# Kernel optimization log

Measured on AMD Instinct MI355X. Metric: run time of the kernel, lower is better.

Reference implementation:

```python
import jax, jax.numpy as jnp
from jax import lax
import numpy as np

B, N = 8192, 4096


def thomas_algorithm(a, b, c, f):
    """Batched Thomas tridiagonal solve.
    a: (B, N-1) sub-diagonal (row i uses a[:, i-1])
    b: (B, N)   diagonal
    c: (B, N-1) super-diagonal (row i uses c[:, i])
    f: (B, N)   rhs
    returns u: (B, N) with A u = f
    """
    Bb = f.shape[0]
    zero_col = jnp.zeros((Bb, 1), dtype=f.dtype)
    a_full = jnp.concatenate([zero_col, a], axis=1)  # (B, N), a_full[:,0] unused (=0)
    c_full = jnp.concatenate([c, zero_col], axis=1)  # (B, N), c_full[:,N-1] unused (=0)

    def fwd_step(carry, inp):
        cp_prev, dp_prev = carry
        ai, bi, ci, fi = inp
        denom = bi - ai * cp_prev
        cp = ci / denom
        dp = (fi - ai * dp_prev) / denom
        return (cp, dp), (cp, dp)

    init = (jnp.zeros(Bb, dtype=f.dtype), jnp.zeros(Bb, dtype=f.dtype))
    xs = (a_full.T, b.T, c_full.T, f.T)  # scan over N, vectorized over B
    _, (cps, dps) = lax.scan(fwd_step, init, xs)

    def bwd_step(u_next, inp):
        cp, dp = inp
        u = dp - cp * u_next
        return u, u

    _, us = lax.scan(bwd_step, jnp.zeros(Bb, dtype=f.dtype), (cps, dps), reverse=True)
    return us.T  # (B, N)


def setup_inputs() -> dict:
    key = jax.random.key(0)
    k1, k2 = jax.random.split(key)
    alpha = jax.random.uniform(k1, (B, N), dtype=jnp.float32)
    f = jax.random.normal(k2, (N,), dtype=jnp.float32)
    return {"alpha": alpha, "f": f}


def reference(alpha, f):
    # f is 1D metadata -> expand to batch, matching torch forward
    f2 = jnp.broadcast_to(f[None, :], alpha.shape)
    # tridiagonal_matrix(alpha)
    a = alpha[:, :-1] ** 2
    b = jnp.maximum(5.0 + alpha ** 3, 0.01)
    c = alpha[:, 1:] ** 2 + 2.0 * alpha[:, 1:]
    u = thomas_algorithm(a, b, c, f2)
    return u
```

## Files before the change

kernel.cpp:

```cpp
#include <hip/hip_runtime.h>


namespace {
constexpr int kCH  = 32;
constexpr int kHL  = 8;
constexpr int kR   = kCH + kHL;
constexpr int kNC  = 128;
constexpr int RPW  = 8;
constexpr int THREADS = 128;
constexpr int F4PR = 69;
constexpr int ST4  = 71;
constexpr int APW4 = RPW * ST4;
constexpr int SF4  = 133;
constexpr int GHI  = 11;
}

using f4v = float __attribute__((ext_vector_type(4)));
using h2v = __fp16 __attribute__((ext_vector_type(2)));

__global__ __launch_bounds__(THREADS, 3) void thomas_v18(
    const float4* __restrict__ alpha4,
    const float4* __restrict__ f4,
    float4* __restrict__ u4)
{
  __shared__ float4 sM[2 * APW4 + SF4];

  const int bid  = blockIdx.x;
  const int pair = bid & 7;
  const int rw0  = (bid >> 3) * RPW;
  const int w    = threadIdx.x >> 6;
  const int lane = threadIdx.x & 63;
  const int j    = lane & 7;
  const int q    = lane >> 3;
  const int cw   = pair * 2 + w;

  float4* __restrict__ sA = sM + w * APW4;
  float4* __restrict__ sF = sM + 2 * APW4;

  {
    const int fb4 = pair * 128 - 3;
    #pragma unroll
    for (int it = 0; it < 3; ++it) {
      const int idx = lane + it * 64;
      if (idx < SF4) {
        int g4 = fb4 + idx;
        g4 = (g4 < 0) ? 0 : ((g4 > 1023) ? 1023 : g4);
        sF[idx] = f4[g4];
      }
    }
  }

  {
    const int cb4 = cw * 64 - 3;
    #pragma unroll 3
    for (int it = 0; it < 9; ++it) {
      int idx = lane + it * 64;
      if (idx > RPW * F4PR - 1) idx = RPW * F4PR - 1;
      const int row = idx / F4PR;
      const int c4  = idx - row * F4PR;
      int g4 = cb4 + c4;
      g4 = (g4 < 0) ? 0 : ((g4 > 1023) ? 1023 : g4);
      sA[row * ST4 + c4] = alpha4[(size_t)(rw0 + row) * 1024 + g4];
    }
  }

#define STEP(am1v, fiv)                                        \
  {                                                            \
    const float c_  = ap1 * (ap1 + 2.0f);                      \
    const float b_  = fmaxf(fmaf(a0 * a0, a0, 5.0f), 0.01f);   \
    const float dn  = fmaf(-c_, ec, b_);                       \
    const float rd  = __builtin_amdgcn_rcpf(dn);               \
    gc = (fiv - c_ * gc) * rd;                                 \
    ec = ((am1v) * (am1v)) * rd;                               \
    ap1 = a0; a0 = (am1v);                                     \
  }

  const int  kk    = cw * 8 + q;
  const bool first = (kk == 0);
  const bool last  = (kk == kNC - 1);
  const int  f4b   = first ? 3 : (q * 8 + 1);
  const int  fOff  = w * 64;
  const float4* __restrict__ A4 = sA + j * ST4;

  h2v gp_pk[kR / 2], ep_pk[kR / 2];
  float ec = 0.0f, gc = 0.0f, ap1 = 0.0f;
  const int ghi = last ? 9 : GHI;
  float4 curA = A4[f4b + ghi];
  float4 lowA = A4[f4b + ghi - 1];
  float4 fcur = sF[fOff + f4b + ghi];
  float4 flow = sF[fOff + f4b + ghi - 1];
  float a0 = curA.w;

  if (!last) {
    #pragma unroll
    for (int g = GHI; g >= 10; --g) {
      const float4 pA = A4[f4b + g - 2];
      const float4 pF = sF[fOff + f4b + g - 2];
      STEP(curA.z, fcur.w)
      STEP(curA.y, fcur.z)
      STEP(curA.x, fcur.y)
      STEP(lowA.w, fcur.x)
      curA = lowA; lowA = pA; fcur = flow; flow = pF;
    }
  }

  #pragma unroll
  for (int g = 9; g >= 0; --g) {
    int pidx = f4b + g - 2;
    if (pidx < 0) pidx = 0;
    const float4 pA = A4[pidx];
    const float4 pF = sF[fOff + pidx];
    float lw = lowA.w;
    if (g == 0 && first) lw = 0.0f;
    STEP(curA.z, fcur.w)  const float g3_ = gc, e3_ = ec;
    STEP(curA.y, fcur.z)  const float g2_ = gc, e2_ = ec;
    STEP(curA.x, fcur.y)  const float g1_ = gc, e1_ = ec;
    STEP(lw,     fcur.x)  const float g0_ = gc, e0_ = ec;
    gp_pk[2 * g + 1] = __builtin_amdgcn_cvt_pkrtz(g2_, g3_);
    gp_pk[2 * g]     = __builtin_amdgcn_cvt_pkrtz(g0_, g1_);
    ep_pk[2 * g + 1] = __builtin_amdgcn_cvt_pkrtz(e2_, e3_);
    ep_pk[2 * g]     = __builtin_amdgcn_cvt_pkrtz(e0_, e1_);
    curA = lowA; lowA = pA; fcur = flow; flow = pF;
  }

  const int tmin = first ? 0 : kHL;
  float up = 0.0f;
  float4 pk;
  #pragma unroll
  for (int t = 0; t < kR; ++t) {
    const float gpv = (float)gp_pk[t >> 1][t & 1];
    const float epv = (float)ep_pk[t >> 1][t & 1];
    const float uv = fmaf(-epv, up, gpv);
    up = uv;
    const int ph = t & 3;
    if      (ph == 0) pk.x = uv;
    else if (ph == 1) pk.y = uv;
    else if (ph == 2) pk.z = uv;
    else {
      pk.w = uv;
      if (t - 3 >= tmin && t < tmin + kCH) {
        sA[j * ST4 + q * 8 + ((t - 3 - tmin) >> 2)] = pk;
      }
    }
  }

  #pragma unroll
  for (int it = 0; it < RPW; ++it) {
    const float4 v = sA[it * ST4 + lane];
    f4v vv; vv.x = v.x; vv.y = v.y; vv.z = v.z; vv.w = v.w;
    __builtin_nontemporal_store(vv, reinterpret_cast<f4v*>(
        u4 + (size_t)(rw0 + it) * 1024 + cw * 64 + lane));
  }

#undef STEP
}

extern "C" void kernel_launch(void* const* d_in, const int* in_sizes, int n_in,
                              void* d_out, int out_size, void* d_ws, size_t ws_size,
                              hipStream_t stream) {
  const float4* alpha = (const float4*)d_in[0];
  const float4* f     = (const float4*)d_in[1];
  float4*       uo    = (float4*)d_out;
  thomas_v18<<<dim3(8192), THREADS, 0, stream>>>(alpha, f, uo);
}
```

Before: 48.20 us.

## Replace per-step reciprocal recurrence with projective (numerator/denominator) form

Rewrites the forward elimination recurrence as a homogeneous linear recurrence in (D, P, N), scaled by 1/8 each step to limit growth. This takes the reciprocal off the loop-carried dependency chain so it becomes an independent op computed only where outputs are needed. The loop-carried path gets shorter, but the per-step FMA count rises and overflow or underflow of the unnormalized D/P over the short window is a numerical risk.

```diff
diff --git a/kernel.cpp b/kernel.cpp
--- a/kernel.cpp
+++ b/kernel.cpp
@@ -18,7 +18,7 @@
 using f4v = float __attribute__((ext_vector_type(4)));
 using h2v = __fp16 __attribute__((ext_vector_type(2)));
 
-__global__ __launch_bounds__(THREADS, 3) void thomas_v18(
+__global__ __launch_bounds__(THREADS, 3) void thomas_v20(
     const float4* __restrict__ alpha4,
     const float4* __restrict__ f4,
     float4* __restrict__ u4)
@@ -64,15 +64,18 @@
     }
   }
 
-#define STEP(am1v, fiv)                                        \
-  {                                                            \
-    const float c_  = ap1 * (ap1 + 2.0f);                      \
-    const float b_  = fmaxf(fmaf(a0 * a0, a0, 5.0f), 0.01f);   \
-    const float dn  = fmaf(-c_, ec, b_);                       \
-    const float rd  = __builtin_amdgcn_rcpf(dn);               \
-    gc = (fiv - c_ * gc) * rd;                                 \
-    ec = ((am1v) * (am1v)) * rd;                               \
-    ap1 = a0; a0 = (am1v);                                     \
+#define MSTEP(am1v, fiv)                                         \
+  {                                                              \
+    const float c8  = ap1 * fmaf(0.125f, ap1, 0.25f);            \
+    const float b8  = fmaxf(fmaf(asq, a0, 5.0f), 0.01f) * 0.125f;\
+    const float nsq = (am1v) * (am1v);                           \
+    const float t1  = c8 * Nc;                                   \
+    const float t2  = (fiv) * 0.125f * Dc;                       \
+    const float Nn  = nsq * 0.125f * Dc;                         \
+    Dc = fmaf(b8, Dc, -t1);                                      \
+    Pc = fmaf(-c8, Pc, t2);                                      \
+    Nc = Nn;                                                     \
+    ap1 = a0; a0 = (am1v); asq = nsq;                            \
   }
 
   const int  kk    = cw * 8 + q;
@@ -83,23 +86,25 @@
   const float4* __restrict__ A4 = sA + j * ST4;
 
   h2v gp_pk[kR / 2], ep_pk[kR / 2];
-  float ec = 0.0f, gc = 0.0f, ap1 = 0.0f;
+  float Dc = 1.0f, Nc = 0.0f, Pc = 0.0f;
+  float ap1 = 0.0f;
   const int ghi = last ? 9 : GHI;
   float4 curA = A4[f4b + ghi];
   float4 lowA = A4[f4b + ghi - 1];
   float4 fcur = sF[fOff + f4b + ghi];
   float4 flow = sF[fOff + f4b + ghi - 1];
-  float a0 = curA.w;
+  float a0  = curA.w;
+  float asq = a0 * a0;
 
   if (!last) {
     #pragma unroll
     for (int g = GHI; g >= 10; --g) {
       const float4 pA = A4[f4b + g - 2];
       const float4 pF = sF[fOff + f4b + g - 2];
-      STEP(curA.z, fcur.w)
-      STEP(curA.y, fcur.z)
-      STEP(curA.x, fcur.y)
-      STEP(lowA.w, fcur.x)
+      MSTEP(curA.z, fcur.w)
+      MSTEP(curA.y, fcur.z)
+      MSTEP(curA.x, fcur.y)
+      MSTEP(lowA.w, fcur.x)
       curA = lowA; lowA = pA; fcur = flow; flow = pF;
     }
   }
@@ -112,10 +117,18 @@
     const float4 pF = sF[fOff + pidx];
     float lw = lowA.w;
     if (g == 0 && first) lw = 0.0f;
-    STEP(curA.z, fcur.w)  const float g3_ = gc, e3_ = ec;
-    STEP(curA.y, fcur.z)  const float g2_ = gc, e2_ = ec;
-    STEP(curA.x, fcur.y)  const float g1_ = gc, e1_ = ec;
-    STEP(lw,     fcur.x)  const float g0_ = gc, e0_ = ec;
+    MSTEP(curA.z, fcur.w)
+    float rd3 = __builtin_amdgcn_rcpf(Dc);
+    const float g3_ = Pc * rd3, e3_ = Nc * rd3;
+    MSTEP(curA.y, fcur.z)
+    float rd2 = __builtin_amdgcn_rcpf(Dc);
+    const float g2_ = Pc * rd2, e2_ = Nc * rd2;
+    MSTEP(curA.x, fcur.y)
+    float rd1 = __builtin_amdgcn_rcpf(Dc);
+    const float g1_ = Pc * rd1, e1_ = Nc * rd1;
+    MSTEP(lw,     fcur.x)
+    float rd0 = __builtin_amdgcn_rcpf(Dc);
+    const float g0_ = Pc * rd0, e0_ = Nc * rd0;
     gp_pk[2 * g + 1] = __builtin_amdgcn_cvt_pkrtz(g2_, g3_);
     gp_pk[2 * g]     = __builtin_amdgcn_cvt_pkrtz(g0_, g1_);
     ep_pk[2 * g + 1] = __builtin_amdgcn_cvt_pkrtz(e2_, e3_);
@@ -152,7 +165,7 @@
         u4 + (size_t)(rw0 + it) * 1024 + cw * 64 + lane));
   }
 
-#undef STEP
+#undef MSTEP
 }
 
 extern "C" void kernel_launch(void* const* d_in, const int* in_sizes, int n_in,
@@ -161,5 +174,5 @@
   const float4* alpha = (const float4*)d_in[0];
   const float4* f     = (const float4*)d_in[1];
   float4*       uo    = (float4*)d_out;
-  thomas_v18<<<dim3(8192), THREADS, 0, stream>>>(alpha, f, uo);
+  thomas_v20<<<dim3(8192), THREADS, 0, stream>>>(alpha, f, uo);
 }
```

After: 49.36 us. +2.4%, slower.
